# Performance work log

Measured on AMD Instinct MI355X. Metric: run time of the kernel, lower is better.

## Reference

```python
import jax, jax.numpy as jnp
import numpy as np

N_NODES = 100000
N_EDGES = 600000
N_GRAPHS = 64
D_IN = 128
D_H = 128


def setup_inputs() -> dict:
    key = jax.random.key(0)
    ks = jax.random.split(key, 12)
    x = jax.random.normal(ks[0], (N_NODES, D_IN), dtype=jnp.float32)
    edge_index = jax.random.randint(ks[1], (2, N_EDGES), 0, N_NODES, dtype=jnp.int64)
    batch = jnp.sort(jax.random.randint(ks[2], (N_NODES,), 0, N_GRAPHS, dtype=jnp.int64))
    s = 1.0 / np.sqrt(D_H)
    W1 = jax.random.normal(ks[3], (D_H, D_IN), dtype=jnp.float32) * s
    W2 = jax.random.normal(ks[4], (D_H, D_H), dtype=jnp.float32) * s
    W3 = jax.random.normal(ks[5], (D_H, D_H), dtype=jnp.float32) * s
    W4 = jax.random.normal(ks[6], (D_H, D_H), dtype=jnp.float32) * s
    Wc = jax.random.normal(ks[7], (1, D_H), dtype=jnp.float32) * s
    b1 = jnp.zeros((D_H,), jnp.float32)
    b2 = jnp.zeros((D_H,), jnp.float32)
    b3 = jnp.zeros((D_H,), jnp.float32)
    b4 = jnp.zeros((D_H,), jnp.float32)
    bc = jnp.zeros((1,), jnp.float32)
    return {"x": x, "edge_index": edge_index, "batch": batch,
            "W1": W1, "b1": b1, "W2": W2, "b2": b2,
            "W3": W3, "b3": b3, "W4": W4, "b4": b4,
            "Wc": Wc, "bc": bc}


def _conv(x, W, b, row, col, n_nodes):
    # Linear transform then sum-aggregate source features at target nodes.
    # (PyG message() returns x_j unscaled -> the degree norm in the original
    # forward is computed but never applied.)
    h = x @ W.T + b                                   # [N, D]
    return jax.ops.segment_sum(h[row], col, num_segments=n_nodes)


def reference(x, edge_index, batch, W1, b1, W2, b2, W3, b3, W4, b4, Wc, bc):
    n = x.shape[0]
    loops = jnp.arange(n, dtype=edge_index.dtype)
    row = jnp.concatenate([edge_index[0], loops])     # sources (with self loops)
    col = jnp.concatenate([edge_index[1], loops])     # targets

    h = jax.nn.relu(_conv(x, W1, b1, row, col, n))    # dropout = identity (eval)
    h = jax.nn.relu(_conv(h, W2, b2, row, col, n))
    h = jax.nn.relu(_conv(h, W3, b3, row, col, n))
    h = _conv(h, W4, b4, row, col, n)

    # global mean pool over graphs
    sums = jax.ops.segment_sum(h, batch, num_segments=N_GRAPHS)        # [G, D]
    cnts = jax.ops.segment_sum(jnp.ones((n,), h.dtype), batch, num_segments=N_GRAPHS)
    pooled = sums / jnp.maximum(cnts, 1.0)[:, None]

    return jax.nn.sigmoid(pooled @ Wc.T + bc)         # [G, 1]
```

## Files before the change

kernel.cpp:

```cpp
#include <hip/hip_runtime.h>
#include <hip/hip_bf16.h>

#define N_NODES 100000
#define N_EDGES 600000
#define N_GRAPHS 64
#define D 128

#define NBLK_SCAN ((N_NODES + 255) / 256)


__global__ void count_deg_k(const int* __restrict__ col, int* __restrict__ cnt) {
    int e = blockIdx.x * blockDim.x + threadIdx.x;
    if (e < N_EDGES) atomicAdd(&cnt[col[e]], 1);
}

__global__ __launch_bounds__(256) void partial_k(const int* __restrict__ cnt,
                                                 int* __restrict__ psum) {
    int i = blockIdx.x * 256 + threadIdx.x;
    int v = (i < N_NODES) ? cnt[i] : 0;
#pragma unroll
    for (int d = 32; d > 0; d >>= 1) v += __shfl_down(v, d, 64);
    __shared__ int ws[4];
    if ((threadIdx.x & 63) == 0) ws[threadIdx.x >> 6] = v;
    __syncthreads();
    if (threadIdx.x == 0) psum[blockIdx.x] = ws[0] + ws[1] + ws[2] + ws[3];
}

__global__ __launch_bounds__(512) void scanpart_k(int* __restrict__ psum) {
    __shared__ int ls[512];
    int t = threadIdx.x;
    int v = (t < NBLK_SCAN) ? psum[t] : 0;
    ls[t] = v;
    __syncthreads();
    for (int d = 1; d < 512; d <<= 1) {
        int u = (t >= d) ? ls[t - d] : 0;
        __syncthreads();
        ls[t] += u;
        __syncthreads();
    }
    if (t < NBLK_SCAN) psum[t] = ls[t] - v;
}

__global__ __launch_bounds__(256) void scan_scatter_k(const int* __restrict__ cnt,
                                                      const int* __restrict__ psum,
                                                      int* __restrict__ start) {
    int b = blockIdx.x, t = threadIdx.x;
    int i = b * 256 + t;
    int v = (i < N_NODES) ? cnt[i] : 0;
    __shared__ int ls[256];
    ls[t] = v;
    __syncthreads();
    for (int d = 1; d < 256; d <<= 1) {
        int u = (t >= d) ? ls[t - d] : 0;
        __syncthreads();
        ls[t] += u;
        __syncthreads();
    }
    int incl = ls[t];
    int off = psum[b];
    if (i < N_NODES) start[i] = off + incl - v;
    if (i == N_NODES - 1) start[N_NODES] = off + incl;
}

__global__ void fill_csr_k(const int* __restrict__ row, const int* __restrict__ col,
                           const int* __restrict__ start, int* __restrict__ fill,
                           int* __restrict__ esrc) {
    int e = blockIdx.x * blockDim.x + threadIdx.x;
    if (e < N_EDGES) {
        int c = col[e];
        int p = atomicAdd(&fill[c], 1);
        esrc[start[c] + p] = row[e];
    }
}


__global__ __launch_bounds__(128) void bounds_k(const int* __restrict__ batch,
                                                int* __restrict__ gstart) {
    int g = threadIdx.x;
    if (g > N_GRAPHS) return;
    int lo = 0, hi = N_NODES;
    while (lo < hi) {
        int mid = (lo + hi) >> 1;
        if (batch[mid] < g) lo = mid + 1; else hi = mid;
    }
    gstart[g] = lo;
}


#define BM 128
#define KT 32

__device__ __forceinline__ void stage32(const float* __restrict__ G, float* lds,
                                        int grow0, int kb, int nrows, int tid) {
    int l = tid & 63, w = tid >> 6;
#pragma unroll
    for (int i = 0; i < 4; ++i) {
        int f = (w + i * 4) * 64 + l;
        int row = f >> 3, c4 = f & 7;
        int s4 = ((row >> 3) ^ row) & 7;
        const float* gp = G + (size_t)(grow0 + row) * D + kb + ((c4 ^ s4) << 2);
        float* lp = lds + (w + i * 4) * 256;
        if (grow0 + row < nrows)
            __builtin_amdgcn_global_load_lds(
                (const __attribute__((address_space(1))) void*)gp,
                (__attribute__((address_space(3))) void*)lp, 16, 0, 0);
    }
}

__global__ __launch_bounds__(256, 2) void gemm_k(const float* __restrict__ A,
                                                 const float* __restrict__ W,
                                                 const float* __restrict__ bias,
                                                 float* __restrict__ out, int nrows) {
    __shared__ float sA[BM * KT];
    __shared__ float sW[BM * KT];
    const int tid = threadIdx.x;
    const int bm0 = blockIdx.x * BM;
    const int tx = tid & 15, ty = tid >> 4;

    float acc[8][8];
#pragma unroll
    for (int i = 0; i < 8; ++i)
#pragma unroll
        for (int r = 0; r < 8; ++r) acc[i][r] = 0.f;

    float bv[8];
#pragma unroll
    for (int r = 0; r < 8; ++r) bv[r] = bias[8 * tx + r];

    for (int kt = 0; kt < D / KT; ++kt) {
        stage32(A, sA, bm0, kt * KT, nrows, tid);
        stage32(W, sW, 0, kt * KT, D, tid);
        __syncthreads();
#pragma unroll
        for (int c4 = 0; c4 < 8; ++c4) {
            float4 a[8], w[8];
#pragma unroll
            for (int i = 0; i < 8; ++i)
                a[i] = *reinterpret_cast<const float4*>(
                    &sA[(8 * ty + i) * KT + ((c4 ^ ((ty ^ i) & 7)) << 2)]);
#pragma unroll
            for (int r = 0; r < 8; ++r)
                w[r] = *reinterpret_cast<const float4*>(
                    &sW[(8 * tx + r) * KT + ((c4 ^ ((tx ^ r) & 7)) << 2)]);
#pragma unroll
            for (int i = 0; i < 8; ++i)
#pragma unroll
                for (int r = 0; r < 8; ++r) {
                    acc[i][r] = fmaf(a[i].x, w[r].x, acc[i][r]);
                    acc[i][r] = fmaf(a[i].y, w[r].y, acc[i][r]);
                    acc[i][r] = fmaf(a[i].z, w[r].z, acc[i][r]);
                    acc[i][r] = fmaf(a[i].w, w[r].w, acc[i][r]);
                }
        }
        __syncthreads();
    }

#pragma unroll
    for (int i = 0; i < 8; ++i) {
        int grow = bm0 + ty * 8 + i;
        if (grow >= nrows) continue;
        float4 o0 = make_float4(acc[i][0] + bv[0], acc[i][1] + bv[1],
                                acc[i][2] + bv[2], acc[i][3] + bv[3]);
        float4 o1 = make_float4(acc[i][4] + bv[4], acc[i][5] + bv[5],
                                acc[i][6] + bv[6], acc[i][7] + bv[7]);
        *reinterpret_cast<float4*>(&out[(size_t)grow * D + tx * 8]) = o0;
        *reinterpret_cast<float4*>(&out[(size_t)grow * D + tx * 8 + 4]) = o1;
    }
}


__global__ __launch_bounds__(256) void aggregate_k(const float* __restrict__ t,
                                                   const int* __restrict__ start,
                                                   const int* __restrict__ esrc,
                                                   float* __restrict__ out, int do_relu) {
    const int wv = threadIdx.x >> 6, l = threadIdx.x & 63;
    const int node = blockIdx.x * 4 + wv;
    if (node >= N_NODES) return;
    const int s = start[node], e = start[node + 1];
    const size_t base = ((size_t)node << 7) + 2 * l;
    float2 acc = *reinterpret_cast<const float2*>(t + base);
    int i = s;
    for (; i + 1 < e; i += 2) {
        const float2 v0 = *reinterpret_cast<const float2*>(t + (((size_t)esrc[i] << 7) + 2 * l));
        const float2 v1 = *reinterpret_cast<const float2*>(t + (((size_t)esrc[i + 1] << 7) + 2 * l));
        acc.x += v0.x + v1.x;
        acc.y += v0.y + v1.y;
    }
    if (i < e) {
        const float2 v = *reinterpret_cast<const float2*>(t + (((size_t)esrc[i] << 7) + 2 * l));
        acc.x += v.x;
        acc.y += v.y;
    }
    if (do_relu) {
        acc.x = fmaxf(acc.x, 0.f);
        acc.y = fmaxf(acc.y, 0.f);
    }
    *reinterpret_cast<float2*>(out + base) = acc;
}


__global__ __launch_bounds__(128) void vbeta_k(const float* __restrict__ W4,
                                               const float* __restrict__ b4,
                                               const float* __restrict__ Wc,
                                               float* __restrict__ vbeta) {
    int k = threadIdx.x;
    float acc = 0.f;
    for (int j = 0; j < D; ++j) acc = fmaf(Wc[j], W4[j * D + k], acc);
    vbeta[k] = acc;
    __shared__ float red[128];
    red[k] = Wc[k] * b4[k];
    __syncthreads();
    for (int st = 64; st > 0; st >>= 1) {
        if (k < st) red[k] += red[k + st];
        __syncthreads();
    }
    if (k == 0) vbeta[D] = red[0];
}

__global__ __launch_bounds__(256) void matvec_k(const float* __restrict__ h,
                                                const float* __restrict__ vbeta,
                                                float* __restrict__ s) {
    int wid = threadIdx.x >> 6, lane = threadIdx.x & 63;
    int row = blockIdx.x * 4 + wid;
    const float2 hv = *reinterpret_cast<const float2*>(&h[(size_t)row * D + lane * 2]);
    const float2 vv = *reinterpret_cast<const float2*>(&vbeta[lane * 2]);
    float dot = fmaf(hv.x, vv.x, hv.y * vv.y);
#pragma unroll
    for (int d = 32; d > 0; d >>= 1) dot += __shfl_down(dot, d, 64);
    if (lane == 0) s[row] = dot;
}

__global__ __launch_bounds__(256) void sagg_k(const float* __restrict__ s,
                                              const int* __restrict__ start,
                                              const int* __restrict__ esrc,
                                              const float* __restrict__ vbeta,
                                              float* __restrict__ a) {
    int i = blockIdx.x * 256 + threadIdx.x;
    if (i >= N_NODES) return;
    int s0 = start[i], s1 = start[i + 1];
    float beta = vbeta[D];
    float acc = s[i] + (float)(1 + s1 - s0) * beta;
    for (int e = s0; e < s1; ++e) acc += s[esrc[e]];
    a[i] = acc;
}

__global__ __launch_bounds__(256) void spool_k(const float* __restrict__ a,
                                               const int* __restrict__ gstart,
                                               const float* __restrict__ bc,
                                               float* __restrict__ out) {
    int g = blockIdx.x;
    int lo = gstart[g], hi = gstart[g + 1];
    float acc = 0.f;
    for (int i = lo + threadIdx.x; i < hi; i += 256) acc += a[i];
    __shared__ float red[256];
    red[threadIdx.x] = acc;
    __syncthreads();
    for (int st = 128; st > 0; st >>= 1) {
        if (threadIdx.x < st) red[threadIdx.x] += red[threadIdx.x + st];
        __syncthreads();
    }
    if (threadIdx.x == 0) {
        float c = (float)max(hi - lo, 1);
        out[g] = 1.f / (1.f + expf(-(red[0] / c + bc[0])));
    }
}


extern "C" void kernel_launch(void* const* d_in, const int* in_sizes, int n_in,
                              void* d_out, int out_size, void* d_ws, size_t ws_size,
                              hipStream_t stream) {
    const float* x   = (const float*)d_in[0];
    const int* ei    = (const int*)d_in[1];
    const int* batch = (const int*)d_in[2];
    const float* W1  = (const float*)d_in[3];
    const float* b1  = (const float*)d_in[4];
    const float* W2  = (const float*)d_in[5];
    const float* b2  = (const float*)d_in[6];
    const float* W3  = (const float*)d_in[7];
    const float* b3  = (const float*)d_in[8];
    const float* W4  = (const float*)d_in[9];
    const float* b4  = (const float*)d_in[10];
    const float* Wc  = (const float*)d_in[11];
    const float* bc  = (const float*)d_in[12];
    float* out = (float*)d_out;

    const int* row = ei;
    const int* col = ei + N_EDGES;

    char* p = (char*)d_ws;
    float* t = (float*)p;      p += (size_t)N_NODES * D * 4;
    float* h = (float*)p;      p += (size_t)N_NODES * D * 4;
    int* esrc = (int*)p;       p += (size_t)N_EDGES * 4;
    int* cstart = (int*)p;     p += ((N_NODES + 1) * 4 + 15) / 16 * 16;
    int* cfill = (int*)p;      p += (size_t)N_NODES * 4;
    int* psum = (int*)p;       p += ((NBLK_SCAN + 3) / 4) * 16;
    int* gstart = (int*)p;     p += 256;

    float* vbeta = t;
    float* s_arr = t + 256;
    float* a_arr = t + 256 + N_NODES;

    hipMemsetAsync(cfill, 0, (size_t)N_NODES * 4, stream);
    count_deg_k<<<(N_EDGES + 255) / 256, 256, 0, stream>>>(col, cfill);
    partial_k<<<NBLK_SCAN, 256, 0, stream>>>(cfill, psum);
    scanpart_k<<<1, 512, 0, stream>>>(psum);
    scan_scatter_k<<<NBLK_SCAN, 256, 0, stream>>>(cfill, psum, cstart);
    hipMemsetAsync(cfill, 0, (size_t)N_NODES * 4, stream);
    fill_csr_k<<<(N_EDGES + 255) / 256, 256, 0, stream>>>(row, col, cstart, cfill, esrc);

    bounds_k<<<1, 128, 0, stream>>>(batch, gstart);

    const int ggrid = (N_NODES + BM - 1) / BM;
    const int agrid = (N_NODES + 3) / 4;

    gemm_k<<<ggrid, 256, 0, stream>>>(x, W1, b1, t, N_NODES);
    aggregate_k<<<agrid, 256, 0, stream>>>(t, cstart, esrc, h, 1);
    gemm_k<<<ggrid, 256, 0, stream>>>(h, W2, b2, t, N_NODES);
    aggregate_k<<<agrid, 256, 0, stream>>>(t, cstart, esrc, h, 1);
    gemm_k<<<ggrid, 256, 0, stream>>>(h, W3, b3, t, N_NODES);
    aggregate_k<<<agrid, 256, 0, stream>>>(t, cstart, esrc, h, 1);

    vbeta_k<<<1, 128, 0, stream>>>(W4, b4, Wc, vbeta);
    matvec_k<<<N_NODES / 4, 256, 0, stream>>>(h, vbeta, s_arr);
    sagg_k<<<(N_NODES + 255) / 256, 256, 0, stream>>>(s_arr, cstart, esrc, vbeta, a_arr);
    spool_k<<<N_GRAPHS, 256, 0, stream>>>(a_arr, gstart, bc, out);
}
```

Baseline: 455.4 us.

## Use split-bf16 MFMA GEMM with hi/lo activation storage

```diff
diff --git a/kernel.cpp b/kernel.cpp
--- a/kernel.cpp
+++ b/kernel.cpp
@@ -7,6 +7,17 @@
 #define D 128
 
 #define NBLK_SCAN ((N_NODES + 255) / 256)
+
+typedef __attribute__((ext_vector_type(8))) short short8v;
+typedef __attribute__((ext_vector_type(4))) float float4v;
+
+__device__ __forceinline__ unsigned short f2bf(float f) {
+    unsigned int u = __float_as_uint(f);
+    return (unsigned short)((u + 0x7FFF + ((u >> 16) & 1)) >> 16);
+}
+__device__ __forceinline__ float bf2f(unsigned short h) {
+    return __uint_as_float(((unsigned int)h) << 16);
+}
 
 
 __global__ void count_deg_k(const int* __restrict__ col, int* __restrict__ cnt) {
@@ -87,84 +98,87 @@
 }
 
 
+__global__ __launch_bounds__(256) void split_k(const float* __restrict__ in,
+                                               unsigned short* __restrict__ hi,
+                                               unsigned short* __restrict__ lo, int n4) {
+    int i = blockIdx.x * 256 + threadIdx.x;
+    if (i >= n4) return;
+    float4 v = reinterpret_cast<const float4*>(in)[i];
+    ushort4 h, l;
+    h.x = f2bf(v.x); l.x = f2bf(v.x - bf2f(h.x));
+    h.y = f2bf(v.y); l.y = f2bf(v.y - bf2f(h.y));
+    h.z = f2bf(v.z); l.z = f2bf(v.z - bf2f(h.z));
+    h.w = f2bf(v.w); l.w = f2bf(v.w - bf2f(h.w));
+    reinterpret_cast<ushort4*>(hi)[i] = h;
+    reinterpret_cast<ushort4*>(lo)[i] = l;
+}
+
+
 #define BM 128
-#define KT 32
-
-__device__ __forceinline__ void stage32(const float* __restrict__ G, float* lds,
-                                        int grow0, int kb, int nrows, int tid) {
-    int l = tid & 63, w = tid >> 6;
-#pragma unroll
-    for (int i = 0; i < 4; ++i) {
-        int f = (w + i * 4) * 64 + l;
-        int row = f >> 3, c4 = f & 7;
-        int s4 = ((row >> 3) ^ row) & 7;
-        const float* gp = G + (size_t)(grow0 + row) * D + kb + ((c4 ^ s4) << 2);
-        float* lp = lds + (w + i * 4) * 256;
-        if (grow0 + row < nrows)
-            __builtin_amdgcn_global_load_lds(
-                (const __attribute__((address_space(1))) void*)gp,
-                (__attribute__((address_space(3))) void*)lp, 16, 0, 0);
-    }
-}
-
-__global__ __launch_bounds__(256, 2) void gemm_k(const float* __restrict__ A,
-                                                 const float* __restrict__ W,
-                                                 const float* __restrict__ bias,
-                                                 float* __restrict__ out, int nrows) {
-    __shared__ float sA[BM * KT];
-    __shared__ float sW[BM * KT];
-    const int tid = threadIdx.x;
+
+__global__ __launch_bounds__(256) void gemm_mfma_k(
+    const unsigned short* __restrict__ Ahi, const unsigned short* __restrict__ Alo,
+    const unsigned short* __restrict__ Whi, const unsigned short* __restrict__ Wlo,
+    const float* __restrict__ bias, float* __restrict__ out, int nrows) {
+    __shared__ float swp[4][32][132];
+    const int tid = threadIdx.x, l = tid & 63, wv = tid >> 6;
     const int bm0 = blockIdx.x * BM;
-    const int tx = tid & 15, ty = tid >> 4;
-
-    float acc[8][8];
-#pragma unroll
-    for (int i = 0; i < 8; ++i)
-#pragma unroll
-        for (int r = 0; r < 8; ++r) acc[i][r] = 0.f;
-
-    float bv[8];
-#pragma unroll
-    for (int r = 0; r < 8; ++r) bv[r] = bias[8 * tx + r];
-
-    for (int kt = 0; kt < D / KT; ++kt) {
-        stage32(A, sA, bm0, kt * KT, nrows, tid);
-        stage32(W, sW, 0, kt * KT, D, tid);
-        __syncthreads();
-#pragma unroll
-        for (int c4 = 0; c4 < 8; ++c4) {
-            float4 a[8], w[8];
-#pragma unroll
-            for (int i = 0; i < 8; ++i)
-                a[i] = *reinterpret_cast<const float4*>(
-                    &sA[(8 * ty + i) * KT + ((c4 ^ ((ty ^ i) & 7)) << 2)]);
-#pragma unroll
-            for (int r = 0; r < 8; ++r)
-                w[r] = *reinterpret_cast<const float4*>(
-                    &sW[(8 * tx + r) * KT + ((c4 ^ ((tx ^ r) & 7)) << 2)]);
-#pragma unroll
-            for (int i = 0; i < 8; ++i)
-#pragma unroll
-                for (int r = 0; r < 8; ++r) {
-                    acc[i][r] = fmaf(a[i].x, w[r].x, acc[i][r]);
-                    acc[i][r] = fmaf(a[i].y, w[r].y, acc[i][r]);
-                    acc[i][r] = fmaf(a[i].z, w[r].z, acc[i][r]);
-                    acc[i][r] = fmaf(a[i].w, w[r].w, acc[i][r]);
-                }
+    const int g = l >> 4, li = l & 15;
+
+    float4v acc[2][8];
+#pragma unroll
+    for (int rg = 0; rg < 2; ++rg)
+#pragma unroll
+        for (int cg = 0; cg < 8; ++cg) acc[rg][cg] = (float4v){0.f, 0.f, 0.f, 0.f};
+
+    size_t abase[2];
+#pragma unroll
+    for (int rg = 0; rg < 2; ++rg)
+        abase[rg] = (size_t)min(bm0 + wv * 32 + rg * 16 + li, nrows - 1) * D + g * 8;
+
+#pragma unroll
+    for (int kk = 0; kk < 4; ++kk) {
+        const int k0 = kk * 32;
+        short8v ah[2], al[2];
+#pragma unroll
+        for (int rg = 0; rg < 2; ++rg) {
+            ah[rg] = *reinterpret_cast<const short8v*>(Ahi + abase[rg] + k0);
+            al[rg] = *reinterpret_cast<const short8v*>(Alo + abase[rg] + k0);
         }
-        __syncthreads();
-    }
-
-#pragma unroll
-    for (int i = 0; i < 8; ++i) {
-        int grow = bm0 + ty * 8 + i;
-        if (grow >= nrows) continue;
-        float4 o0 = make_float4(acc[i][0] + bv[0], acc[i][1] + bv[1],
-                                acc[i][2] + bv[2], acc[i][3] + bv[3]);
-        float4 o1 = make_float4(acc[i][4] + bv[4], acc[i][5] + bv[5],
-                                acc[i][6] + bv[6], acc[i][7] + bv[7]);
-        *reinterpret_cast<float4*>(&out[(size_t)grow * D + tx * 8]) = o0;
-        *reinterpret_cast<float4*>(&out[(size_t)grow * D + tx * 8 + 4]) = o1;
+#pragma unroll
+        for (int cg = 0; cg < 8; ++cg) {
+            const size_t wb = (size_t)(cg * 16 + li) * D + g * 8 + k0;
+            short8v wh = *reinterpret_cast<const short8v*>(Whi + wb);
+            short8v wl = *reinterpret_cast<const short8v*>(Wlo + wb);
+#pragma unroll
+            for (int rg = 0; rg < 2; ++rg) {
+                acc[rg][cg] = __builtin_amdgcn_mfma_f32_16x16x32_bf16(ah[rg], wh, acc[rg][cg], 0, 0, 0);
+                acc[rg][cg] = __builtin_amdgcn_mfma_f32_16x16x32_bf16(al[rg], wh, acc[rg][cg], 0, 0, 0);
+                acc[rg][cg] = __builtin_amdgcn_mfma_f32_16x16x32_bf16(ah[rg], wl, acc[rg][cg], 0, 0, 0);
+                acc[rg][cg] = __builtin_amdgcn_mfma_f32_16x16x32_bf16(al[rg], wl, acc[rg][cg], 0, 0, 0);
+            }
+        }
+    }
+
+#pragma unroll
+    for (int rg = 0; rg < 2; ++rg)
+#pragma unroll
+        for (int cg = 0; cg < 8; ++cg)
+#pragma unroll
+            for (int r = 0; r < 4; ++r)
+                swp[wv][rg * 16 + g * 4 + r][cg * 16 + li] = acc[rg][cg][r];
+
+    const int c4 = l & 31, rh = l >> 5;
+    const float4 bias_v = *reinterpret_cast<const float4*>(&bias[c4 * 4]);
+#pragma unroll
+    for (int it = 0; it < 16; ++it) {
+        int rowl = it * 2 + rh;
+        int grow = bm0 + wv * 32 + rowl;
+        if (grow < nrows) {
+            float4 v = *reinterpret_cast<const float4*>(&swp[wv][rowl][c4 * 4]);
+            v.x += bias_v.x; v.y += bias_v.y; v.z += bias_v.z; v.w += bias_v.w;
+            *reinterpret_cast<float4*>(&out[(size_t)grow * D + c4 * 4]) = v;
+        }
     }
 }
 
@@ -172,7 +186,9 @@
 __global__ __launch_bounds__(256) void aggregate_k(const float* __restrict__ t,
                                                    const int* __restrict__ start,
                                                    const int* __restrict__ esrc,
-                                                   float* __restrict__ out, int do_relu) {
+                                                   unsigned short* __restrict__ ohi,
+                                                   unsigned short* __restrict__ olo,
+                                                   int do_relu) {
     const int wv = threadIdx.x >> 6, l = threadIdx.x & 63;
     const int node = blockIdx.x * 4 + wv;
     if (node >= N_NODES) return;
@@ -195,7 +211,10 @@
         acc.x = fmaxf(acc.x, 0.f);
         acc.y = fmaxf(acc.y, 0.f);
     }
-    *reinterpret_cast<float2*>(out + base) = acc;
+    unsigned short hx = f2bf(acc.x), hy = f2bf(acc.y);
+    unsigned short lx = f2bf(acc.x - bf2f(hx)), ly = f2bf(acc.y - bf2f(hy));
+    *reinterpret_cast<unsigned int*>(ohi + base) = (unsigned int)hx | ((unsigned int)hy << 16);
+    *reinterpret_cast<unsigned int*>(olo + base) = (unsigned int)lx | ((unsigned int)ly << 16);
 }
 
 
@@ -217,14 +236,19 @@
     if (k == 0) vbeta[D] = red[0];
 }
 
-__global__ __launch_bounds__(256) void matvec_k(const float* __restrict__ h,
+__global__ __launch_bounds__(256) void matvec_k(const unsigned short* __restrict__ hhi,
+                                                const unsigned short* __restrict__ hlo,
                                                 const float* __restrict__ vbeta,
                                                 float* __restrict__ s) {
     int wid = threadIdx.x >> 6, lane = threadIdx.x & 63;
     int row = blockIdx.x * 4 + wid;
-    const float2 hv = *reinterpret_cast<const float2*>(&h[(size_t)row * D + lane * 2]);
+    const size_t base = (size_t)row * D + lane * 2;
+    unsigned int h2 = *reinterpret_cast<const unsigned int*>(hhi + base);
+    unsigned int l2 = *reinterpret_cast<const unsigned int*>(hlo + base);
+    float hx = bf2f((unsigned short)h2) + bf2f((unsigned short)l2);
+    float hy = bf2f((unsigned short)(h2 >> 16)) + bf2f((unsigned short)(l2 >> 16));
     const float2 vv = *reinterpret_cast<const float2*>(&vbeta[lane * 2]);
-    float dot = fmaf(hv.x, vv.x, hv.y * vv.y);
+    float dot = fmaf(hx, vv.x, hy * vv.y);
 #pragma unroll
     for (int d = 32; d > 0; d >>= 1) dot += __shfl_down(dot, d, 64);
     if (lane == 0) s[row] = dot;
@@ -288,13 +312,16 @@
     const int* col = ei + N_EDGES;
 
     char* p = (char*)d_ws;
-    float* t = (float*)p;      p += (size_t)N_NODES * D * 4;
-    float* h = (float*)p;      p += (size_t)N_NODES * D * 4;
-    int* esrc = (int*)p;       p += (size_t)N_EDGES * 4;
-    int* cstart = (int*)p;     p += ((N_NODES + 1) * 4 + 15) / 16 * 16;
-    int* cfill = (int*)p;      p += (size_t)N_NODES * 4;
-    int* psum = (int*)p;       p += ((NBLK_SCAN + 3) / 4) * 16;
-    int* gstart = (int*)p;     p += 256;
+    float* t = (float*)p;            p += (size_t)N_NODES * D * 4;
+    unsigned short* hhi = (unsigned short*)p; p += (size_t)N_NODES * D * 2;
+    unsigned short* hlo = (unsigned short*)p; p += (size_t)N_NODES * D * 2;
+    unsigned short* whi = (unsigned short*)p; p += (size_t)D * D * 2;
+    unsigned short* wlo = (unsigned short*)p; p += (size_t)D * D * 2;
+    int* esrc = (int*)p;             p += (size_t)N_EDGES * 4;
+    int* cstart = (int*)p;           p += ((N_NODES + 1) * 4 + 15) / 16 * 16;
+    int* cfill = (int*)p;            p += (size_t)N_NODES * 4;
+    int* psum = (int*)p;             p += ((NBLK_SCAN + 3) / 4) * 16;
+    int* gstart = (int*)p;           p += 256;
 
     float* vbeta = t;
     float* s_arr = t + 256;
@@ -312,16 +339,22 @@
 
     const int ggrid = (N_NODES + BM - 1) / BM;
     const int agrid = (N_NODES + 3) / 4;
-
-    gemm_k<<<ggrid, 256, 0, stream>>>(x, W1, b1, t, N_NODES);
-    aggregate_k<<<agrid, 256, 0, stream>>>(t, cstart, esrc, h, 1);
-    gemm_k<<<ggrid, 256, 0, stream>>>(h, W2, b2, t, N_NODES);
-    aggregate_k<<<agrid, 256, 0, stream>>>(t, cstart, esrc, h, 1);
-    gemm_k<<<ggrid, 256, 0, stream>>>(h, W3, b3, t, N_NODES);
-    aggregate_k<<<agrid, 256, 0, stream>>>(t, cstart, esrc, h, 1);
+    const int xn4 = N_NODES * D / 4;
+    const int wn4 = D * D / 4;
+
+    split_k<<<(xn4 + 255) / 256, 256, 0, stream>>>(x, hhi, hlo, xn4);
+    split_k<<<(wn4 + 255) / 256, 256, 0, stream>>>(W1, whi, wlo, wn4);
+    gemm_mfma_k<<<ggrid, 256, 0, stream>>>(hhi, hlo, whi, wlo, b1, t, N_NODES);
+    aggregate_k<<<agrid, 256, 0, stream>>>(t, cstart, esrc, hhi, hlo, 1);
+    split_k<<<(wn4 + 255) / 256, 256, 0, stream>>>(W2, whi, wlo, wn4);
+    gemm_mfma_k<<<ggrid, 256, 0, stream>>>(hhi, hlo, whi, wlo, b2, t, N_NODES);
+    aggregate_k<<<agrid, 256, 0, stream>>>(t, cstart, esrc, hhi, hlo, 1);
+    split_k<<<(wn4 + 255) / 256, 256, 0, stream>>>(W3, whi, wlo, wn4);
+    gemm_mfma_k<<<ggrid, 256, 0, stream>>>(hhi, hlo, whi, wlo, b3, t, N_NODES);
+    aggregate_k<<<agrid, 256, 0, stream>>>(t, cstart, esrc, hhi, hlo, 1);
 
     vbeta_k<<<1, 128, 0, stream>>>(W4, b4, Wc, vbeta);
-    matvec_k<<<N_NODES / 4, 256, 0, stream>>>(h, vbeta, s_arr);
+    matvec_k<<<N_NODES / 4, 256, 0, stream>>>(hhi, hlo, vbeta, s_arr);
     sagg_k<<<(N_NODES + 255) / 256, 256, 0, stream>>>(s_arr, cstart, esrc, vbeta, a_arr);
     spool_k<<<N_GRAPHS, 256, 0, stream>>>(a_arr, gstart, bc, out);
 }
```

Result: faster. 443.2 us (-2.7%).
